# Optimization experiments

Measured on AMD Instinct MI355X. Metric: run time of the kernel, lower is better.

Reference implementation:

```python
import jax, jax.numpy as jnp
import numpy as np

N, E, D, H, K = 8192, 8, 1024, 4096, 2


def setup_inputs() -> dict:
    key = jax.random.key(0)
    ks = jax.random.split(key, 12)
    s = 0.02  # init scale for weights
    return {
        "x": jax.random.normal(ks[0], (N, D), jnp.float32),
        "noise": jax.random.normal(ks[1], (N, E), jnp.float32),
        "Wg_w": jax.random.normal(ks[2], (D, E), jnp.float32) * s,
        "Wg_b": jnp.zeros((E,), jnp.float32),
        "Wn_w": jax.random.normal(ks[3], (D, E), jnp.float32) * s,
        "Wn_b": jnp.zeros((E,), jnp.float32),
        "w1": jax.random.normal(ks[4], (E, D, H), jnp.float32) * s,
        "b1": jnp.zeros((E, H), jnp.float32),
        "w2": jax.random.normal(ks[5], (E, H, D), jnp.float32) * s,
        "b2": jnp.zeros((E, D), jnp.float32),
        "k": K,
    }


def reference(x, noise, Wg_w, Wg_b, Wn_w, Wn_b, w1, b1, w2, b2, k):
    # --- noisy top-k gating: H(x) = Wg(x) + noise * softplus(Wn(x)) ---
    g_logits = x @ Wg_w + Wg_b                       # [N, E]
    n_scale = jax.nn.softplus(x @ Wn_w + Wn_b)       # [N, E]
    h = g_logits + noise * n_scale                   # [N, E]
    topk_vals, topk_inds = jax.lax.top_k(h, k)       # [N, k]
    gates = jax.nn.softmax(topk_vals, axis=-1)       # [N, k]

    # Scatter top-k gates into a dense [N, E] map (zeros for unselected experts),
    # so the weighted combine is exactly sum_j gates[n,j] * expert_{inds[n,j]}(x_n).
    n_tok, n_exp = h.shape
    dense_gates = jnp.zeros((n_tok, n_exp), h.dtype).at[
        jnp.arange(n_tok)[:, None], topk_inds
    ].set(gates)                                     # [N, E]

    # --- per-expert 2-layer MLP: fc2(relu(fc1(x))) ---
    hid = jax.nn.relu(jnp.einsum('nd,edh->neh', x, w1) + b1)  # [N, E, H]
    y = jnp.einsum('neh,ehd->ned', hid, w2) + b2              # [N, E, D]
    out = jnp.einsum('ned,ne->nd', y, dense_gates)            # [N, D]
    return out
```

## Files before the change

### kernel.cpp

```cpp
#include <hip/hip_runtime.h>
#include <hip/hip_bf16.h>

#define NTOK 8192
#define NEXP 8
#define DMODEL 1024
#define DHID 4096

typedef __bf16 bf16x8 __attribute__((ext_vector_type(8)));
typedef float f32x4 __attribute__((ext_vector_type(4)));

__device__ __forceinline__ unsigned short f2bf(float f) {
  return __builtin_bit_cast(unsigned short, __float2bfloat16(f));
}

__device__ __forceinline__ void gload_lds16(const void* g, void* l) {
  __builtin_amdgcn_global_load_lds(
      (const __attribute__((address_space(1))) unsigned int*)g,
      (__attribute__((address_space(3))) unsigned int*)l, 16, 0, 0);
}

__device__ __forceinline__ int imin(int a, int b) { return a < b ? a : b; }

constexpr size_t OFF_XB   = 0;
constexpr size_t OFF_W1T  = OFF_XB + (size_t)NTOK * DMODEL * 2;
constexpr size_t OFF_W2T  = OFF_W1T + (size_t)NEXP * DHID * DMODEL * 2;
constexpr size_t OFF_HID  = OFF_W2T + (size_t)NEXP * DMODEL * DHID * 2;
constexpr size_t OFF_IDX  = OFF_HID + (size_t)NTOK * 2 * DHID * 2;
constexpr size_t OFF_GATE = OFF_IDX + (size_t)NTOK * 2 * 4;
constexpr size_t OFF_LIST = OFF_GATE + (size_t)NTOK * 2 * 4;
constexpr size_t OFF_CNT  = OFF_LIST + (size_t)NTOK * 2 * 4;
constexpr size_t OFF_OFFS = OFF_CNT + 128;
constexpr size_t OFF_CUR  = OFF_OFFS + 128;

__global__ void convert_x_kernel(const float4* __restrict__ in,
                                 ushort4* __restrict__ out, int n4) {
  int i = blockIdx.x * 256 + threadIdx.x;
  if (i < n4) {
    float4 v = in[i];
    ushort4 o;
    o.x = f2bf(v.x); o.y = f2bf(v.y); o.z = f2bf(v.z); o.w = f2bf(v.w);
    out[i] = o;
  }
}

__global__ void transpose_bf16_kernel(const float* __restrict__ in,
                                      unsigned short* __restrict__ out,
                                      int R, int C) {
  __shared__ float sh[64][65];
  const size_t ebase = (size_t)blockIdx.z * R * C;
  const float* ine = in + ebase;
  unsigned short* oute = out + ebase;
  int c0 = blockIdx.x * 64, r0 = blockIdx.y * 64;
  int tx = threadIdx.x & 15, ty = threadIdx.x >> 4;
#pragma unroll
  for (int p = 0; p < 4; ++p) {
    int row = ty + p * 16;
    float4 v = *(const float4*)&ine[(size_t)(r0 + row) * C + c0 + tx * 4];
    sh[row][tx * 4 + 0] = v.x;
    sh[row][tx * 4 + 1] = v.y;
    sh[row][tx * 4 + 2] = v.z;
    sh[row][tx * 4 + 3] = v.w;
  }
  __syncthreads();
#pragma unroll
  for (int p = 0; p < 4; ++p) {
    int crow = ty + p * 16;
    ushort4 o;
    o.x = f2bf(sh[tx * 4 + 0][crow]);
    o.y = f2bf(sh[tx * 4 + 1][crow]);
    o.z = f2bf(sh[tx * 4 + 2][crow]);
    o.w = f2bf(sh[tx * 4 + 3][crow]);
    *(ushort4*)&oute[(size_t)(c0 + crow) * R + r0 + tx * 4] = o;
  }
}

__global__ void gating_kernel(const float* __restrict__ x,
                              const float* __restrict__ noise,
                              const float* __restrict__ Wg_w,
                              const float* __restrict__ Wg_b,
                              const float* __restrict__ Wn_w,
                              const float* __restrict__ Wn_b,
                              int* __restrict__ topk_idx,
                              float* __restrict__ topk_gate,
                              int* __restrict__ counts) {
  int wave = threadIdx.x >> 6;
  int lane = threadIdx.x & 63;
  int n = blockIdx.x * 4 + wave;
  if (n >= NTOK) return;

  float ag[8] = {0.f, 0.f, 0.f, 0.f, 0.f, 0.f, 0.f, 0.f};
  float an[8] = {0.f, 0.f, 0.f, 0.f, 0.f, 0.f, 0.f, 0.f};
  const float* xr = x + (size_t)n * DMODEL;
#pragma unroll 4
  for (int i = 0; i < DMODEL / 64; ++i) {
    int d = lane + i * 64;
    float xv = xr[d];
    const float4* wg = (const float4*)(Wg_w + (size_t)d * 8);
    const float4* wn = (const float4*)(Wn_w + (size_t)d * 8);
    float4 g0 = wg[0], g1 = wg[1];
    float4 n0 = wn[0], n1 = wn[1];
    ag[0] += xv * g0.x; ag[1] += xv * g0.y; ag[2] += xv * g0.z; ag[3] += xv * g0.w;
    ag[4] += xv * g1.x; ag[5] += xv * g1.y; ag[6] += xv * g1.z; ag[7] += xv * g1.w;
    an[0] += xv * n0.x; an[1] += xv * n0.y; an[2] += xv * n0.z; an[3] += xv * n0.w;
    an[4] += xv * n1.x; an[5] += xv * n1.y; an[6] += xv * n1.z; an[7] += xv * n1.w;
  }
#pragma unroll
  for (int off = 32; off > 0; off >>= 1) {
#pragma unroll
    for (int j = 0; j < 8; ++j) {
      ag[j] += __shfl_down(ag[j], off, 64);
      an[j] += __shfl_down(an[j], off, 64);
    }
  }
  if (lane == 0) {
    float h[8];
#pragma unroll
    for (int e = 0; e < 8; ++e) {
      float gl = ag[e] + Wg_b[e];
      float z = an[e] + Wn_b[e];
      float sp = fmaxf(z, 0.f) + log1pf(expf(-fabsf(z)));
      h[e] = gl + noise[(size_t)n * 8 + e] * sp;
    }
    int i0 = 0; float v0 = h[0];
#pragma unroll
    for (int e = 1; e < 8; ++e)
      if (h[e] > v0) { v0 = h[e]; i0 = e; }
    int i1 = -1; float v1 = -1e30f;
#pragma unroll
    for (int e = 0; e < 8; ++e)
      if (e != i0 && h[e] > v1) { v1 = h[e]; i1 = e; }
    float e1 = expf(v1 - v0);
    float inv = 1.f / (1.f + e1);
    topk_idx[n * 2] = i0;
    topk_idx[n * 2 + 1] = i1;
    topk_gate[n * 2] = inv;
    topk_gate[n * 2 + 1] = e1 * inv;
    atomicAdd(&counts[i0], 1);
    atomicAdd(&counts[i1], 1);
  }
}

__global__ void scan_kernel(const int* __restrict__ counts,
                            int* __restrict__ offsets, int* __restrict__ cursor) {
  if (threadIdx.x == 0) {
    int acc = 0;
    for (int e = 0; e < NEXP; ++e) {
      offsets[e] = acc;
      cursor[e] = acc;
      acc += counts[e];
    }
    offsets[NEXP] = acc;
  }
}

__global__ void scatter_kernel(const int* __restrict__ topk_idx,
                               int* __restrict__ cursor, int* __restrict__ list) {
  int n = blockIdx.x * 256 + threadIdx.x;
  if (n >= NTOK) return;
#pragma unroll
  for (int j = 0; j < 2; ++j) {
    int e = topk_idx[n * 2 + j];
    int pos = atomicAdd(&cursor[e], 1);
    list[pos] = n * 2 + j;
  }
}

template <int MODE>
__global__ __launch_bounds__(256) void expert_gemm(
    const unsigned short* __restrict__ Asrc, const unsigned short* __restrict__ Bt,
    const float* __restrict__ bias, const int* __restrict__ offsets,
    const int* __restrict__ list, const float* __restrict__ gates,
    unsigned short* __restrict__ hid, float* __restrict__ out) {
  constexpr int K = MODE ? DHID : DMODEL;
  constexpr int Nout = MODE ? DMODEL : DHID;

  const int gx = gridDim.x;
  const int lin = blockIdx.x + gx * (blockIdx.y + 64 * blockIdx.z);
  const int e = lin & 7;
  const int r = lin >> 3;
  const int by = r & 63;
  const int bx = r >> 6;

  const int off = offsets[e];
  const int ne = offsets[e + 1] - off;
  const int m0 = by * 128;
  if (m0 >= ne) return;
  const int n0 = bx * 128;

  __shared__ alignas(16) unsigned short Alds[128 * 32];
  __shared__ alignas(16) unsigned short Blds[128 * 32];

  const int tid = threadIdx.x;
  const int lane = tid & 63;
  const int w = tid >> 6;
  const int wm = (w >> 1) * 64;
  const int wn = (w & 1) * 64;
  const int lr = lane & 15;
  const int kg = lane >> 4;

  const unsigned short* srcA[2];
  const unsigned short* srcB[2];
#pragma unroll
  for (int i = 0; i < 2; ++i) {
    int q = tid + i * 256;
    int rr = q >> 2, c = q & 3;
    int p = off + imin(m0 + rr, ne - 1);
    if (MODE == 0) {
      int token = list[p] >> 1;
      srcA[i] = Asrc + (size_t)token * DMODEL + c * 8;
    } else {
      srcA[i] = Asrc + (size_t)p * DHID + c * 8;
    }
    srcB[i] = Bt + (size_t)e * Nout * K + (size_t)(n0 + rr) * K + c * 8;
  }

  f32x4 acc[4][4] = {};

  for (int kt = 0; kt < K; kt += 32) {
#pragma unroll
    for (int i = 0; i < 2; ++i) {
      int q = tid + i * 256;
      gload_lds16(srcA[i] + kt, &Alds[q * 8]);
      gload_lds16(srcB[i] + kt, &Blds[q * 8]);
    }
    __syncthreads();

    bf16x8 af[4], bfr[4];
#pragma unroll
    for (int mf = 0; mf < 4; ++mf)
      af[mf] = *(const bf16x8*)&Alds[(wm + mf * 16 + lr) * 32 + kg * 8];
#pragma unroll
    for (int nf = 0; nf < 4; ++nf)
      bfr[nf] = *(const bf16x8*)&Blds[(wn + nf * 16 + lr) * 32 + kg * 8];
#pragma unroll
    for (int mf = 0; mf < 4; ++mf)
#pragma unroll
      for (int nf = 0; nf < 4; ++nf)
        acc[mf][nf] = __builtin_amdgcn_mfma_f32_16x16x32_bf16(af[mf], bfr[nf],
                                                              acc[mf][nf], 0, 0, 0);
    __syncthreads();
  }

  if (MODE == 0) {
#pragma unroll
    for (int mf = 0; mf < 4; ++mf) {
#pragma unroll
      for (int i = 0; i < 4; ++i) {
        int rloc = wm + mf * 16 + kg * 4 + i;
        int row = m0 + rloc;
        if (row < ne) {
          size_t p = (size_t)(off + row);
#pragma unroll
          for (int nf = 0; nf < 4; ++nf) {
            int col = n0 + wn + nf * 16 + lr;
            float v = acc[mf][nf][i] + bias[(size_t)e * Nout + col];
            v = fmaxf(v, 0.f);
            hid[p * DHID + col] = f2bf(v);
          }
        }
      }
    }
  } else {
#pragma unroll
    for (int mf = 0; mf < 4; ++mf) {
#pragma unroll
      for (int i = 0; i < 4; ++i) {
        int rloc = wm + mf * 16 + kg * 4 + i;
        int row = m0 + rloc;
        if (row < ne) {
          int lv = list[off + row];
          int token = lv >> 1;
          float g = gates[lv];
#pragma unroll
          for (int nf = 0; nf < 4; ++nf) {
            int col = n0 + wn + nf * 16 + lr;
            float v = (acc[mf][nf][i] + bias[(size_t)e * Nout + col]) * g;
            atomicAdd(&out[(size_t)token * DMODEL + col], v);
          }
        }
      }
    }
  }
}

extern "C" void kernel_launch(void* const* d_in, const int* in_sizes, int n_in,
                              void* d_out, int out_size, void* d_ws, size_t ws_size,
                              hipStream_t stream) {
  const float* x = (const float*)d_in[0];
  const float* noise = (const float*)d_in[1];
  const float* Wg_w = (const float*)d_in[2];
  const float* Wg_b = (const float*)d_in[3];
  const float* Wn_w = (const float*)d_in[4];
  const float* Wn_b = (const float*)d_in[5];
  const float* w1 = (const float*)d_in[6];
  const float* b1 = (const float*)d_in[7];
  const float* w2 = (const float*)d_in[8];
  const float* b2 = (const float*)d_in[9];
  float* out = (float*)d_out;

  char* ws = (char*)d_ws;
  unsigned short* xb = (unsigned short*)(ws + OFF_XB);
  unsigned short* w1t = (unsigned short*)(ws + OFF_W1T);
  unsigned short* w2t = (unsigned short*)(ws + OFF_W2T);
  unsigned short* hid = (unsigned short*)(ws + OFF_HID);
  int* topk_idx = (int*)(ws + OFF_IDX);
  float* topk_gate = (float*)(ws + OFF_GATE);
  int* list = (int*)(ws + OFF_LIST);
  int* counts = (int*)(ws + OFF_CNT);
  int* offsets = (int*)(ws + OFF_OFFS);
  int* cursor = (int*)(ws + OFF_CUR);

  hipMemsetAsync(out, 0, (size_t)NTOK * DMODEL * sizeof(float), stream);
  hipMemsetAsync(counts, 0, NEXP * sizeof(int), stream);

  {
    int n4 = NTOK * DMODEL / 4;
    convert_x_kernel<<<(n4 + 255) / 256, 256, 0, stream>>>((const float4*)x,
                                                           (ushort4*)xb, n4);
  }
  transpose_bf16_kernel<<<dim3(DHID / 64, DMODEL / 64, NEXP), 256, 0, stream>>>(
      w1, w1t, DMODEL, DHID);
  transpose_bf16_kernel<<<dim3(DMODEL / 64, DHID / 64, NEXP), 256, 0, stream>>>(
      w2, w2t, DHID, DMODEL);

  gating_kernel<<<NTOK / 4, 256, 0, stream>>>(x, noise, Wg_w, Wg_b, Wn_w, Wn_b,
                                              topk_idx, topk_gate, counts);
  scan_kernel<<<1, 64, 0, stream>>>(counts, offsets, cursor);
  scatter_kernel<<<NTOK / 256, 256, 0, stream>>>(topk_idx, cursor, list);

  expert_gemm<0><<<dim3(DHID / 128, 64, NEXP), 256, 0, stream>>>(
      xb, w1t, b1, offsets, list, topk_gate, hid, nullptr);
  expert_gemm<1><<<dim3(DMODEL / 128, 64, NEXP), 256, 0, stream>>>(
      hid, w2t, b2, offsets, list, topk_gate, nullptr, out);
}
```

Before: 893.0 us.

## Double-buffer expert GEMM LDS tiles, swizzle LDS chunks, fuse x conversion into gating

The expert GEMM now uses two LDS buffers, so the global-to-LDS load of the next K tile is issued before the MFMAs on the current tile, and one barrier per iteration is dropped. The 16-byte chunk column is XOR-swizzled by row both when loading into LDS and when reading fragments, to reduce LDS bank conflicts. The separate fp32-to-bf16 conversion of x is folded into the gating kernel, which already reads x, removing one kernel launch and one full pass over x. LDS use doubles per block, which may lower occupancy, and the bf16 stores in the gating kernel are 2-byte scattered writes.

```diff
diff --git a/kernel.cpp b/kernel.cpp
--- a/kernel.cpp
+++ b/kernel.cpp
@@ -32,17 +32,6 @@
 constexpr size_t OFF_OFFS = OFF_CNT + 128;
 constexpr size_t OFF_CUR  = OFF_OFFS + 128;
 
-__global__ void convert_x_kernel(const float4* __restrict__ in,
-                                 ushort4* __restrict__ out, int n4) {
-  int i = blockIdx.x * 256 + threadIdx.x;
-  if (i < n4) {
-    float4 v = in[i];
-    ushort4 o;
-    o.x = f2bf(v.x); o.y = f2bf(v.y); o.z = f2bf(v.z); o.w = f2bf(v.w);
-    out[i] = o;
-  }
-}
-
 __global__ void transpose_bf16_kernel(const float* __restrict__ in,
                                       unsigned short* __restrict__ out,
                                       int R, int C) {
@@ -80,6 +69,7 @@
                               const float* __restrict__ Wg_b,
                               const float* __restrict__ Wn_w,
                               const float* __restrict__ Wn_b,
+                              unsigned short* __restrict__ xb,
                               int* __restrict__ topk_idx,
                               float* __restrict__ topk_gate,
                               int* __restrict__ counts) {
@@ -91,10 +81,12 @@
   float ag[8] = {0.f, 0.f, 0.f, 0.f, 0.f, 0.f, 0.f, 0.f};
   float an[8] = {0.f, 0.f, 0.f, 0.f, 0.f, 0.f, 0.f, 0.f};
   const float* xr = x + (size_t)n * DMODEL;
+  unsigned short* xbr = xb + (size_t)n * DMODEL;
 #pragma unroll 4
   for (int i = 0; i < DMODEL / 64; ++i) {
     int d = lane + i * 64;
     float xv = xr[d];
+    xbr[d] = f2bf(xv);
     const float4* wg = (const float4*)(Wg_w + (size_t)d * 8);
     const float4* wn = (const float4*)(Wn_w + (size_t)d * 8);
     float4 g0 = wg[0], g1 = wg[1];
@@ -173,6 +165,7 @@
     unsigned short* __restrict__ hid, float* __restrict__ out) {
   constexpr int K = MODE ? DHID : DMODEL;
   constexpr int Nout = MODE ? DMODEL : DHID;
+  constexpr int NT = K / 32;
 
   const int gx = gridDim.x;
   const int lin = blockIdx.x + gx * (blockIdx.y + 64 * blockIdx.z);
@@ -187,8 +180,8 @@
   if (m0 >= ne) return;
   const int n0 = bx * 128;
 
-  __shared__ alignas(16) unsigned short Alds[128 * 32];
-  __shared__ alignas(16) unsigned short Blds[128 * 32];
+  __shared__ alignas(16) unsigned short Al[2][128 * 32];
+  __shared__ alignas(16) unsigned short Bl[2][128 * 32];
 
   const int tid = threadIdx.x;
   const int lane = tid & 63;
@@ -197,6 +190,7 @@
   const int wn = (w & 1) * 64;
   const int lr = lane & 15;
   const int kg = lane >> 4;
+  const int chrd = ((kg ^ (lr & 3)) * 8);
 
   const unsigned short* srcA[2];
   const unsigned short* srcB[2];
@@ -204,58 +198,68 @@
   for (int i = 0; i < 2; ++i) {
     int q = tid + i * 256;
     int rr = q >> 2, c = q & 3;
+    int cs = c ^ (rr & 3);
     int p = off + imin(m0 + rr, ne - 1);
     if (MODE == 0) {
       int token = list[p] >> 1;
-      srcA[i] = Asrc + (size_t)token * DMODEL + c * 8;
+      srcA[i] = Asrc + (size_t)token * DMODEL + cs * 8;
     } else {
-      srcA[i] = Asrc + (size_t)p * DHID + c * 8;
-    }
-    srcB[i] = Bt + (size_t)e * Nout * K + (size_t)(n0 + rr) * K + c * 8;
+      srcA[i] = Asrc + (size_t)p * DHID + cs * 8;
+    }
+    srcB[i] = Bt + (size_t)e * Nout * K + (size_t)(n0 + rr) * K + cs * 8;
   }
 
   f32x4 acc[4][4] = {};
 
-  for (int kt = 0; kt < K; kt += 32) {
+  auto stage = [&](int buf, int kt) {
 #pragma unroll
     for (int i = 0; i < 2; ++i) {
       int q = tid + i * 256;
-      gload_lds16(srcA[i] + kt, &Alds[q * 8]);
-      gload_lds16(srcB[i] + kt, &Blds[q * 8]);
-    }
-    __syncthreads();
-
+      gload_lds16(srcA[i] + kt * 32, &Al[buf][q * 8]);
+      gload_lds16(srcB[i] + kt * 32, &Bl[buf][q * 8]);
+    }
+  };
+
+  auto compute = [&](int buf) {
     bf16x8 af[4], bfr[4];
 #pragma unroll
     for (int mf = 0; mf < 4; ++mf)
-      af[mf] = *(const bf16x8*)&Alds[(wm + mf * 16 + lr) * 32 + kg * 8];
+      af[mf] = *(const bf16x8*)&Al[buf][(wm + mf * 16 + lr) * 32 + chrd];
 #pragma unroll
     for (int nf = 0; nf < 4; ++nf)
-      bfr[nf] = *(const bf16x8*)&Blds[(wn + nf * 16 + lr) * 32 + kg * 8];
+      bfr[nf] = *(const bf16x8*)&Bl[buf][(wn + nf * 16 + lr) * 32 + chrd];
 #pragma unroll
     for (int mf = 0; mf < 4; ++mf)
 #pragma unroll
       for (int nf = 0; nf < 4; ++nf)
         acc[mf][nf] = __builtin_amdgcn_mfma_f32_16x16x32_bf16(af[mf], bfr[nf],
                                                               acc[mf][nf], 0, 0, 0);
+  };
+
+  stage(0, 0);
+  __syncthreads();
+  int cur = 0;
+  for (int t = 0; t < NT; ++t) {
+    if (t + 1 < NT) stage(cur ^ 1, t + 1);
+    compute(cur);
     __syncthreads();
+    cur ^= 1;
   }
 
   if (MODE == 0) {
 #pragma unroll
     for (int mf = 0; mf < 4; ++mf) {
 #pragma unroll
-      for (int i = 0; i < 4; ++i) {
-        int rloc = wm + mf * 16 + kg * 4 + i;
+      for (int j = 0; j < 4; ++j) {
+        int rloc = wm + mf * 16 + kg * 4 + j;
         int row = m0 + rloc;
         if (row < ne) {
           size_t p = (size_t)(off + row);
 #pragma unroll
           for (int nf = 0; nf < 4; ++nf) {
             int col = n0 + wn + nf * 16 + lr;
-            float v = acc[mf][nf][i] + bias[(size_t)e * Nout + col];
-            v = fmaxf(v, 0.f);
-            hid[p * DHID + col] = f2bf(v);
+            float v = acc[mf][nf][j] + bias[(size_t)e * Nout + col];
+            hid[p * DHID + col] = f2bf(fmaxf(v, 0.f));
           }
         }
       }
@@ -264,8 +268,8 @@
 #pragma unroll
     for (int mf = 0; mf < 4; ++mf) {
 #pragma unroll
-      for (int i = 0; i < 4; ++i) {
-        int rloc = wm + mf * 16 + kg * 4 + i;
+      for (int j = 0; j < 4; ++j) {
+        int rloc = wm + mf * 16 + kg * 4 + j;
         int row = m0 + rloc;
         if (row < ne) {
           int lv = list[off + row];
@@ -274,7 +278,7 @@
 #pragma unroll
           for (int nf = 0; nf < 4; ++nf) {
             int col = n0 + wn + nf * 16 + lr;
-            float v = (acc[mf][nf][i] + bias[(size_t)e * Nout + col]) * g;
+            float v = (acc[mf][nf][j] + bias[(size_t)e * Nout + col]) * g;
             atomicAdd(&out[(size_t)token * DMODEL + col], v);
           }
         }
@@ -313,18 +317,13 @@
   hipMemsetAsync(out, 0, (size_t)NTOK * DMODEL * sizeof(float), stream);
   hipMemsetAsync(counts, 0, NEXP * sizeof(int), stream);
 
-  {
-    int n4 = NTOK * DMODEL / 4;
-    convert_x_kernel<<<(n4 + 255) / 256, 256, 0, stream>>>((const float4*)x,
-                                                           (ushort4*)xb, n4);
-  }
   transpose_bf16_kernel<<<dim3(DHID / 64, DMODEL / 64, NEXP), 256, 0, stream>>>(
       w1, w1t, DMODEL, DHID);
   transpose_bf16_kernel<<<dim3(DMODEL / 64, DHID / 64, NEXP), 256, 0, stream>>>(
       w2, w2t, DHID, DMODEL);
 
   gating_kernel<<<NTOK / 4, 256, 0, stream>>>(x, noise, Wg_w, Wg_b, Wn_w, Wn_b,
-                                              topk_idx, topk_gate, counts);
+                                              xb, topk_idx, topk_gate, counts);
   scan_kernel<<<1, 64, 0, stream>>>(counts, offsets, cursor);
   scatter_kernel<<<NTOK / 256, 256, 0, stream>>>(topk_idx, cursor, list);
 
```

Measured after the change: 913.9 us. 2.3% more time.
